# Optimization experiments

Measured on AMD Instinct MI355X. Metric: run time of the kernel, lower is better.

The kernel has to match this reference:

```python
import jax, jax.numpy as jnp
import numpy as np

N = 131072
K = 1024
D = 64

def setup_inputs() -> dict:
    key = jax.random.key(0)
    k1, k2 = jax.random.split(key)
    x = jax.random.normal(k1, (N, D), dtype=jnp.float32)
    emb_weight = jax.random.normal(k2, (K, D), dtype=jnp.float32)
    return {"x": x, "emb_weight": emb_weight}

def reference(x, emb_weight):
    distances = (
        jnp.sum(x * x, axis=1, keepdims=True)
        + jnp.sum(emb_weight * emb_weight, axis=1)
        - 2.0 * jnp.matmul(x, emb_weight.T)
    )
    codebook_indices = jnp.argmin(distances, axis=1)  # [N]
    probs = jax.nn.one_hot(codebook_indices, K, dtype=x.dtype)  # [N, K]
    z_q = emb_weight[codebook_indices]  # [N, D]
    return (z_q, probs)
```

## Files before the change

kernel.cpp:

```cpp
#include <hip/hip_runtime.h>
#include <math.h>

#define N_TOK 131072
#define K_CB  1024
#define D_DIM 64
#define MARGIN 0.0625f

#define WS_EN     0
#define WS_ES     4096
#define WS_CNT    266240
#define WS_LIST   266248

typedef short bf16x8 __attribute__((ext_vector_type(8)));
typedef float f32x4  __attribute__((ext_vector_type(4)));

__device__ __forceinline__ ushort f2bf(float f) {
    uint u = __float_as_uint(f);
    u += 0x7FFFu + ((u >> 16) & 1u);
    return (ushort)(u >> 16);
}
__device__ __forceinline__ float bf2f(ushort h) {
    return __uint_as_float(((uint)h) << 16);
}

__global__ __launch_bounds__(256) void prep_kernel(
    const float* __restrict__ emb, float* __restrict__ en,
    ushort* __restrict__ es, uint* __restrict__ fixcnt)
{
    const int tid = threadIdx.x;
    const int pb  = blockIdx.x;
    const int c6  = tid & 63;
    const int q   = tid >> 6;
    const int code = pb * 64 + c6;
    if (pb == 0 && tid == 0) *fixcnt = 0;

    const int cb = code >> 4, jj = code & 15;
    const float* er = emb + (size_t)code * D_DIM;
    #pragma unroll
    for (int j = 0; j < 16; ++j) {
        int d = q * 16 + j;
        float f = er[d];
        ushort h = f2bf(f);
        ushort l = f2bf(f - bf2f(h));
        int ks = d >> 5, quad = (d >> 3) & 3, e = d & 7;
        es[(size_t)(((cb * 4 + ks)     * 4 + quad) * 16 + jj) * 8 + e] = h;
        es[(size_t)(((cb * 4 + ks + 2) * 4 + quad) * 16 + jj) * 8 + e] = l;
    }
    if (q == 0) {
        float s = 0.f;
        #pragma unroll
        for (int d = 0; d < D_DIM; ++d) s = fmaf(er[d], er[d], s);
        en[code] = s;
    }
}

__global__ __launch_bounds__(256) void vq_onehot(
    const float* __restrict__ x, const float* __restrict__ emb,
    const float* __restrict__ en, const ushort* __restrict__ es,
    float* __restrict__ zq, float* __restrict__ probs,
    uint* __restrict__ fixcnt, uint* __restrict__ fixlist, uint fixcap)
{
    const int tid  = threadIdx.x;
    const int wave = tid >> 6, lane = tid & 63;
    const int quad = lane >> 4, l15 = lane & 15;
    const int waveRow = blockIdx.x * 128 + wave * 32;

    __shared__ int lds_bk[128];

    bf16x8 af[2][4];
    #pragma unroll
    for (int g = 0; g < 2; ++g) {
        const float* xr = x + (size_t)(waveRow + g * 16 + l15) * D_DIM + quad * 8;
        f32x4 p0 = *(const f32x4*)(xr);
        f32x4 p1 = *(const f32x4*)(xr + 4);
        f32x4 p2 = *(const f32x4*)(xr + 32);
        f32x4 p3 = *(const f32x4*)(xr + 36);
        float v0[8], v1[8];
        #pragma unroll
        for (int j = 0; j < 4; ++j) { v0[j] = p0[j]; v0[4 + j] = p1[j]; v1[j] = p2[j]; v1[4 + j] = p3[j]; }
        #pragma unroll
        for (int j = 0; j < 8; ++j) {
            ushort h0 = f2bf(v0[j]);
            af[g][0][j] = (short)h0;
            af[g][2][j] = (short)f2bf(v0[j] - bf2f(h0));
            ushort h1 = f2bf(v1[j]);
            af[g][1][j] = (short)h1;
            af[g][3][j] = (short)f2bf(v1[j] - bf2f(h1));
        }
    }

    float b1[8], b2[8]; int k1[8];
    #pragma unroll
    for (int s = 0; s < 8; ++s) { b1[s] = INFINITY; b2[s] = INFINITY; k1[s] = 0; }

    const bf16x8* __restrict__ esv = (const bf16x8*)es;
    const int fidx = quad * 16 + l15;

    bf16x8 bc[4]; float enc;
    #pragma unroll
    for (int ks = 0; ks < 4; ++ks) bc[ks] = esv[ks * 64 + fidx];
    enc = en[l15];

    #pragma unroll 2
    for (int cb = 0; cb < 64; ++cb) {
        const int nb = (cb + 1) & 63;
        bf16x8 bn[4]; float enn;
        #pragma unroll
        for (int ks = 0; ks < 4; ++ks) bn[ks] = esv[(size_t)nb * 256 + ks * 64 + fidx];
        enn = en[nb * 16 + l15];

        f32x4 acc0 = {0.f, 0.f, 0.f, 0.f};
        f32x4 acc1 = {0.f, 0.f, 0.f, 0.f};
        acc0 = __builtin_amdgcn_mfma_f32_16x16x32_bf16(af[0][0], bc[0], acc0, 0, 0, 0);
        acc0 = __builtin_amdgcn_mfma_f32_16x16x32_bf16(af[0][1], bc[1], acc0, 0, 0, 0);
        acc0 = __builtin_amdgcn_mfma_f32_16x16x32_bf16(af[0][0], bc[2], acc0, 0, 0, 0);
        acc0 = __builtin_amdgcn_mfma_f32_16x16x32_bf16(af[0][1], bc[3], acc0, 0, 0, 0);
        acc0 = __builtin_amdgcn_mfma_f32_16x16x32_bf16(af[0][2], bc[0], acc0, 0, 0, 0);
        acc0 = __builtin_amdgcn_mfma_f32_16x16x32_bf16(af[0][3], bc[1], acc0, 0, 0, 0);
        acc1 = __builtin_amdgcn_mfma_f32_16x16x32_bf16(af[1][0], bc[0], acc1, 0, 0, 0);
        acc1 = __builtin_amdgcn_mfma_f32_16x16x32_bf16(af[1][1], bc[1], acc1, 0, 0, 0);
        acc1 = __builtin_amdgcn_mfma_f32_16x16x32_bf16(af[1][0], bc[2], acc1, 0, 0, 0);
        acc1 = __builtin_amdgcn_mfma_f32_16x16x32_bf16(af[1][1], bc[3], acc1, 0, 0, 0);
        acc1 = __builtin_amdgcn_mfma_f32_16x16x32_bf16(af[1][2], bc[0], acc1, 0, 0, 0);
        acc1 = __builtin_amdgcn_mfma_f32_16x16x32_bf16(af[1][3], bc[1], acc1, 0, 0, 0);

        const int code = cb * 16 + l15;
        #pragma unroll
        for (int r = 0; r < 4; ++r) {
            {
                float d = fmaf(-2.f, acc0[r], enc);
                bool lt = d < b1[r];
                b2[r] = lt ? b1[r] : fminf(b2[r], d);
                k1[r] = lt ? code : k1[r];
                b1[r] = lt ? d : b1[r];
            }
            {
                int s = 4 + r;
                float d = fmaf(-2.f, acc1[r], enc);
                bool lt = d < b1[s];
                b2[s] = lt ? b1[s] : fminf(b2[s], d);
                k1[s] = lt ? code : k1[s];
                b1[s] = lt ? d : b1[s];
            }
        }

        #pragma unroll
        for (int ks = 0; ks < 4; ++ks) bc[ks] = bn[ks];
        enc = enn;
    }

    #pragma unroll
    for (int s = 0; s < 8; ++s) {
        #pragma unroll
        for (int off = 1; off < 16; off <<= 1) {
            float ob1 = __shfl_xor(b1[s], off);
            int   ok1 = __shfl_xor(k1[s], off);
            float ob2 = __shfl_xor(b2[s], off);
            bool better = (ob1 < b1[s]) || (ob1 == b1[s] && ok1 < k1[s]);
            float loser = better ? b1[s] : ob1;
            b1[s] = better ? ob1 : b1[s];
            k1[s] = better ? ok1 : k1[s];
            b2[s] = fminf(fminf(b2[s], ob2), loser);
        }
    }

    if (l15 == 0) {
        #pragma unroll
        for (int s = 0; s < 8; ++s) {
            int lrow = wave * 32 + (s >> 2) * 16 + quad * 4 + (s & 3);
            lds_bk[lrow] = k1[s];
            if (b2[s] - b1[s] <= MARGIN) {
                uint idx = atomicAdd(fixcnt, 1u);
                if (idx < fixcap)
                    fixlist[idx] = (uint)(blockIdx.x * 128 + lrow) | ((uint)k1[s] << 17);
            }
        }
    }

    #pragma unroll
    for (int mb = 0; mb < 8; ++mb) {
        int bk = lds_bk[wave * 32 + mb * 4 + quad];
        f32x4 v = ((const f32x4*)(emb + (size_t)bk * D_DIM))[l15];
        ((f32x4*)(zq + (size_t)(waveRow + mb * 4 + quad) * D_DIM))[l15] = v;
    }

    for (int m = 0; m < 32; ++m) {
        int bk = lds_bk[wave * 32 + m];
        float* prow = probs + (size_t)(waveRow + m) * K_CB;
        #pragma unroll
        for (int s = 0; s < 4; ++s) {
            int c = s * 256 + lane * 4;
            f32x4 v;
            v[0] = (c     == bk) ? 1.f : 0.f;
            v[1] = (c + 1 == bk) ? 1.f : 0.f;
            v[2] = (c + 2 == bk) ? 1.f : 0.f;
            v[3] = (c + 3 == bk) ? 1.f : 0.f;
            __builtin_nontemporal_store(v, (f32x4*)(prow + c));
        }
    }
}

__global__ __launch_bounds__(256) void vq_fixup(
    const float* __restrict__ x, const float* __restrict__ emb,
    const float* __restrict__ en,
    float* __restrict__ zq, float* __restrict__ probs,
    const uint* __restrict__ fixcnt, const uint* __restrict__ fixlist, uint fixcap)
{
    const int lane = threadIdx.x & 63;
    const uint gwave = (uint)((blockIdx.x * 256 + threadIdx.x) >> 6);
    uint cnt = *fixcnt;
    if (cnt > fixcap) cnt = fixcap;

    for (uint e = gwave; e < cnt; e += 1024u) {
        uint w = fixlist[e];
        int row = (int)(w & 0x1FFFFu);
        int kg  = (int)(w >> 17);
        const float* xr = x + (size_t)row * D_DIM;
        float xn = 0.f;
        #pragma unroll
        for (int d = 0; d < D_DIM; ++d) xn = fmaf(xr[d], xr[d], xn);

        float bd = INFINITY; int bk = 0;
        for (int t = 0; t < 16; ++t) {
            int code = t * 64 + lane;
            const float* er = emb + (size_t)code * D_DIM;
            float a0 = 0.f, a1 = 0.f, a2 = 0.f, a3 = 0.f;
            #pragma unroll
            for (int d = 0; d < D_DIM; d += 4) {
                a0 = fmaf(xr[d + 0], er[d + 0], a0);
                a1 = fmaf(xr[d + 1], er[d + 1], a1);
                a2 = fmaf(xr[d + 2], er[d + 2], a2);
                a3 = fmaf(xr[d + 3], er[d + 3], a3);
            }
            float acc = (a0 + a1) + (a2 + a3);
            float dist = fmaf(-2.f, acc, xn + en[code]);
            if (dist < bd) { bd = dist; bk = code; }
        }
        #pragma unroll
        for (int off = 1; off < 64; off <<= 1) {
            float od = __shfl_xor(bd, off);
            int   ok = __shfl_xor(bk, off);
            if (od < bd || (od == bd && ok < bk)) { bd = od; bk = ok; }
        }
        if (bk != kg) {
            if (lane == 0) {
                probs[(size_t)row * K_CB + kg] = 0.f;
                probs[(size_t)row * K_CB + bk] = 1.f;
            }
            if (lane < 16)
                ((f32x4*)(zq + (size_t)row * D_DIM))[lane] =
                    ((const f32x4*)(emb + (size_t)bk * D_DIM))[lane];
        }
    }
}

extern "C" void kernel_launch(void* const* d_in, const int* in_sizes, int n_in,
                              void* d_out, int out_size, void* d_ws, size_t ws_size,
                              hipStream_t stream) {
    const float* x   = (const float*)d_in[0];
    const float* emb = (const float*)d_in[1];
    float* zq    = (float*)d_out;
    float* probs = (float*)d_out + (size_t)N_TOK * D_DIM;

    char* ws = (char*)d_ws;
    float*  en      = (float*)(ws + WS_EN);
    ushort* es      = (ushort*)(ws + WS_ES);
    uint*   fixcnt  = (uint*)(ws + WS_CNT);
    uint*   fixlist = (uint*)(ws + WS_LIST);
    uint fixcap = (ws_size > WS_LIST + 4) ? (uint)((ws_size - WS_LIST) / 4) : 0u;

    prep_kernel<<<16, 256, 0, stream>>>(emb, en, es, fixcnt);
    vq_onehot<<<N_TOK / 128, 256, 0, stream>>>(x, emb, en, es, zq, probs, fixcnt, fixlist, fixcap);
    vq_fixup<<<256, 256, 0, stream>>>(x, emb, en, zq, probs, fixcnt, fixlist, fixcap);
}
```

Measured before the change: 661.2 us.

## Split one-hot probs writing into a separate streaming kernel

```diff
diff --git a/kernel.cpp b/kernel.cpp
--- a/kernel.cpp
+++ b/kernel.cpp
@@ -9,7 +9,8 @@
 #define WS_EN     0
 #define WS_ES     4096
 #define WS_CNT    266240
-#define WS_LIST   266248
+#define WS_BK     266256
+#define WS_LIST   790544
 
 typedef short bf16x8 __attribute__((ext_vector_type(8)));
 typedef float f32x4  __attribute__((ext_vector_type(4)));
@@ -54,16 +55,17 @@
     }
 }
 
-__global__ __launch_bounds__(256) void vq_onehot(
+__global__ __launch_bounds__(256) void vq_compute(
     const float* __restrict__ x, const float* __restrict__ emb,
     const float* __restrict__ en, const ushort* __restrict__ es,
-    float* __restrict__ zq, float* __restrict__ probs,
+    float* __restrict__ zq, int* __restrict__ bklist,
     uint* __restrict__ fixcnt, uint* __restrict__ fixlist, uint fixcap)
 {
     const int tid  = threadIdx.x;
     const int wave = tid >> 6, lane = tid & 63;
     const int quad = lane >> 4, l15 = lane & 15;
-    const int waveRow = blockIdx.x * 128 + wave * 32;
+    const int blockRow = blockIdx.x * 128;
+    const int waveRow  = blockRow + wave * 32;
 
     __shared__ int lds_bk[128];
 
@@ -169,10 +171,11 @@
         for (int s = 0; s < 8; ++s) {
             int lrow = wave * 32 + (s >> 2) * 16 + quad * 4 + (s & 3);
             lds_bk[lrow] = k1[s];
+            bklist[blockRow + lrow] = k1[s];
             if (b2[s] - b1[s] <= MARGIN) {
                 uint idx = atomicAdd(fixcnt, 1u);
                 if (idx < fixcap)
-                    fixlist[idx] = (uint)(blockIdx.x * 128 + lrow) | ((uint)k1[s] << 17);
+                    fixlist[idx] = (uint)(blockRow + lrow) | ((uint)k1[s] << 17);
             }
         }
     }
@@ -183,20 +186,25 @@
         f32x4 v = ((const f32x4*)(emb + (size_t)bk * D_DIM))[l15];
         ((f32x4*)(zq + (size_t)(waveRow + mb * 4 + quad) * D_DIM))[l15] = v;
     }
-
-    for (int m = 0; m < 32; ++m) {
-        int bk = lds_bk[wave * 32 + m];
-        float* prow = probs + (size_t)(waveRow + m) * K_CB;
-        #pragma unroll
-        for (int s = 0; s < 4; ++s) {
-            int c = s * 256 + lane * 4;
-            f32x4 v;
-            v[0] = (c     == bk) ? 1.f : 0.f;
-            v[1] = (c + 1 == bk) ? 1.f : 0.f;
-            v[2] = (c + 2 == bk) ? 1.f : 0.f;
-            v[3] = (c + 3 == bk) ? 1.f : 0.f;
-            __builtin_nontemporal_store(v, (f32x4*)(prow + c));
-        }
+}
+
+__global__ __launch_bounds__(256) void onehot_writer(
+    const int* __restrict__ bklist, float* __restrict__ probs)
+{
+    const int tid = threadIdx.x;
+    const int blk = blockIdx.x;
+    const int c   = tid * 4;
+    f32x4* p = (f32x4*)probs + (size_t)blk * 16384 + tid;
+    const int* bkp = bklist + blk * 64;
+    #pragma unroll
+    for (int i = 0; i < 64; ++i) {
+        const int bk = bkp[i];
+        f32x4 v;
+        v[0] = (c     == bk) ? 1.f : 0.f;
+        v[1] = (c + 1 == bk) ? 1.f : 0.f;
+        v[2] = (c + 2 == bk) ? 1.f : 0.f;
+        v[3] = (c + 3 == bk) ? 1.f : 0.f;
+        p[(size_t)i * 256] = v;
     }
 }
 
@@ -266,10 +274,12 @@
     float*  en      = (float*)(ws + WS_EN);
     ushort* es      = (ushort*)(ws + WS_ES);
     uint*   fixcnt  = (uint*)(ws + WS_CNT);
+    int*    bklist  = (int*)(ws + WS_BK);
     uint*   fixlist = (uint*)(ws + WS_LIST);
     uint fixcap = (ws_size > WS_LIST + 4) ? (uint)((ws_size - WS_LIST) / 4) : 0u;
 
     prep_kernel<<<16, 256, 0, stream>>>(emb, en, es, fixcnt);
-    vq_onehot<<<N_TOK / 128, 256, 0, stream>>>(x, emb, en, es, zq, probs, fixcnt, fixlist, fixcap);
+    vq_compute<<<N_TOK / 128, 256, 0, stream>>>(x, emb, en, es, zq, bklist, fixcnt, fixlist, fixcap);
+    onehot_writer<<<N_TOK / 64, 256, 0, stream>>>(bklist, probs);
     vq_fixup<<<256, 256, 0, stream>>>(x, emb, en, zq, probs, fixcnt, fixlist, fixcap);
 }
```

New measurement: 699.3 us. 1.06x slower.

## Split codebook across wave pairs and vectorize fixup distance search

Applied to the files above, without the earlier changes.

```diff
diff --git a/kernel.cpp b/kernel.cpp
--- a/kernel.cpp
+++ b/kernel.cpp
@@ -4,12 +4,12 @@
 #define N_TOK 131072
 #define K_CB  1024
 #define D_DIM 64
-#define MARGIN 0.0625f
+#define MARGIN 0.03f
 
 #define WS_EN     0
 #define WS_ES     4096
 #define WS_CNT    266240
-#define WS_LIST   266248
+#define WS_LIST   266256
 
 typedef short bf16x8 __attribute__((ext_vector_type(8)));
 typedef float f32x4  __attribute__((ext_vector_type(4)));
@@ -63,14 +63,20 @@
     const int tid  = threadIdx.x;
     const int wave = tid >> 6, lane = tid & 63;
     const int quad = lane >> 4, l15 = lane & 15;
-    const int waveRow = blockIdx.x * 128 + wave * 32;
-
-    __shared__ int lds_bk[128];
+    const int rg = wave >> 1;
+    const int h  = wave & 1;
+    const int blockRow = blockIdx.x * 64;
+    const int waveRowBase = blockRow + rg * 32;
+
+    __shared__ float lds_b1[2][64];
+    __shared__ float lds_b2[2][64];
+    __shared__ int   lds_k1[2][64];
+    __shared__ int   lds_bk[64];
 
     bf16x8 af[2][4];
     #pragma unroll
     for (int g = 0; g < 2; ++g) {
-        const float* xr = x + (size_t)(waveRow + g * 16 + l15) * D_DIM + quad * 8;
+        const float* xr = x + (size_t)(waveRowBase + g * 16 + l15) * D_DIM + quad * 8;
         f32x4 p0 = *(const f32x4*)(xr);
         f32x4 p1 = *(const f32x4*)(xr + 4);
         f32x4 p2 = *(const f32x4*)(xr + 32);
@@ -95,19 +101,21 @@
 
     const bf16x8* __restrict__ esv = (const bf16x8*)es;
     const int fidx = quad * 16 + l15;
+    const int cb0  = h * 32;
 
     bf16x8 bc[4]; float enc;
     #pragma unroll
-    for (int ks = 0; ks < 4; ++ks) bc[ks] = esv[ks * 64 + fidx];
-    enc = en[l15];
+    for (int ks = 0; ks < 4; ++ks) bc[ks] = esv[(size_t)cb0 * 256 + ks * 64 + fidx];
+    enc = en[cb0 * 16 + l15];
 
     #pragma unroll 2
-    for (int cb = 0; cb < 64; ++cb) {
-        const int nb = (cb + 1) & 63;
+    for (int i = 0; i < 32; ++i) {
+        const int cb  = cb0 + i;
+        const int nbi = cb0 + ((i + 1) & 31);
         bf16x8 bn[4]; float enn;
         #pragma unroll
-        for (int ks = 0; ks < 4; ++ks) bn[ks] = esv[(size_t)nb * 256 + ks * 64 + fidx];
-        enn = en[nb * 16 + l15];
+        for (int ks = 0; ks < 4; ++ks) bn[ks] = esv[(size_t)nbi * 256 + ks * 64 + fidx];
+        enn = en[nbi * 16 + l15];
 
         f32x4 acc0 = {0.f, 0.f, 0.f, 0.f};
         f32x4 acc1 = {0.f, 0.f, 0.f, 0.f};
@@ -167,26 +175,42 @@
     if (l15 == 0) {
         #pragma unroll
         for (int s = 0; s < 8; ++s) {
-            int lrow = wave * 32 + (s >> 2) * 16 + quad * 4 + (s & 3);
-            lds_bk[lrow] = k1[s];
-            if (b2[s] - b1[s] <= MARGIN) {
-                uint idx = atomicAdd(fixcnt, 1u);
-                if (idx < fixcap)
-                    fixlist[idx] = (uint)(blockIdx.x * 128 + lrow) | ((uint)k1[s] << 17);
-            }
-        }
-    }
-
-    #pragma unroll
-    for (int mb = 0; mb < 8; ++mb) {
-        int bk = lds_bk[wave * 32 + mb * 4 + quad];
+            int idx = rg * 32 + (s >> 2) * 16 + quad * 4 + (s & 3);
+            lds_b1[h][idx] = b1[s];
+            lds_b2[h][idx] = b2[s];
+            lds_k1[h][idx] = k1[s];
+        }
+    }
+    __syncthreads();
+
+    if (tid < 64) {
+        float a1 = lds_b1[0][tid], a2 = lds_b2[0][tid]; int ak = lds_k1[0][tid];
+        float c1 = lds_b1[1][tid], c2 = lds_b2[1][tid]; int ck = lds_k1[1][tid];
+        bool bwin = c1 < a1;
+        float m1 = bwin ? c1 : a1;
+        int   mk = bwin ? ck : ak;
+        float loser = bwin ? a1 : c1;
+        float m2 = fminf(fminf(a2, c2), loser);
+        lds_bk[tid] = mk;
+        if (m2 - m1 <= MARGIN) {
+            uint idx = atomicAdd(fixcnt, 1u);
+            if (idx < fixcap) fixlist[idx] = (uint)(blockRow + tid) | ((uint)mk << 17);
+        }
+    }
+    __syncthreads();
+
+    #pragma unroll
+    for (int mb = 0; mb < 4; ++mb) {
+        int rl = wave * 16 + mb * 4 + quad;
+        int bk = lds_bk[rl];
         f32x4 v = ((const f32x4*)(emb + (size_t)bk * D_DIM))[l15];
-        ((f32x4*)(zq + (size_t)(waveRow + mb * 4 + quad) * D_DIM))[l15] = v;
-    }
-
-    for (int m = 0; m < 32; ++m) {
-        int bk = lds_bk[wave * 32 + m];
-        float* prow = probs + (size_t)(waveRow + m) * K_CB;
+        ((f32x4*)(zq + (size_t)(blockRow + rl) * D_DIM))[l15] = v;
+    }
+
+    for (int m = 0; m < 16; ++m) {
+        int rl = wave * 16 + m;
+        int bk = lds_bk[rl];
+        float* prow = probs + (size_t)(blockRow + rl) * K_CB;
         #pragma unroll
         for (int s = 0; s < 4; ++s) {
             int c = s * 256 + lane * 4;
@@ -195,7 +219,7 @@
             v[1] = (c + 1 == bk) ? 1.f : 0.f;
             v[2] = (c + 2 == bk) ? 1.f : 0.f;
             v[3] = (c + 3 == bk) ? 1.f : 0.f;
-            __builtin_nontemporal_store(v, (f32x4*)(prow + c));
+            *(f32x4*)(prow + c) = v;
         }
     }
 }
@@ -207,6 +231,7 @@
     const uint* __restrict__ fixcnt, const uint* __restrict__ fixlist, uint fixcap)
 {
     const int lane = threadIdx.x & 63;
+    const int quad = lane >> 4, l15 = lane & 15;
     const uint gwave = (uint)((blockIdx.x * 256 + threadIdx.x) >> 6);
     uint cnt = *fixcnt;
     if (cnt > fixcap) cnt = fixcap;
@@ -215,29 +240,37 @@
         uint w = fixlist[e];
         int row = (int)(w & 0x1FFFFu);
         int kg  = (int)(w >> 17);
-        const float* xr = x + (size_t)row * D_DIM;
+
+        const f32x4* xr4 = (const f32x4*)(x + (size_t)row * D_DIM) + quad * 4;
+        f32x4 xv[4];
+        #pragma unroll
+        for (int c = 0; c < 4; ++c) xv[c] = xr4[c];
         float xn = 0.f;
         #pragma unroll
-        for (int d = 0; d < D_DIM; ++d) xn = fmaf(xr[d], xr[d], xn);
+        for (int c = 0; c < 4; ++c)
+            #pragma unroll
+            for (int j = 0; j < 4; ++j) xn = fmaf(xv[c][j], xv[c][j], xn);
+        xn += __shfl_xor(xn, 16);
+        xn += __shfl_xor(xn, 32);
 
         float bd = INFINITY; int bk = 0;
-        for (int t = 0; t < 16; ++t) {
-            int code = t * 64 + lane;
-            const float* er = emb + (size_t)code * D_DIM;
-            float a0 = 0.f, a1 = 0.f, a2 = 0.f, a3 = 0.f;
+        for (int t = 0; t < 64; ++t) {
+            int code = t * 16 + l15;
+            const f32x4* er4 = (const f32x4*)(emb + (size_t)code * D_DIM) + quad * 4;
+            float dot = 0.f;
             #pragma unroll
-            for (int d = 0; d < D_DIM; d += 4) {
-                a0 = fmaf(xr[d + 0], er[d + 0], a0);
-                a1 = fmaf(xr[d + 1], er[d + 1], a1);
-                a2 = fmaf(xr[d + 2], er[d + 2], a2);
-                a3 = fmaf(xr[d + 3], er[d + 3], a3);
+            for (int c = 0; c < 4; ++c) {
+                f32x4 ev = er4[c];
+                #pragma unroll
+                for (int j = 0; j < 4; ++j) dot = fmaf(xv[c][j], ev[j], dot);
             }
-            float acc = (a0 + a1) + (a2 + a3);
-            float dist = fmaf(-2.f, acc, xn + en[code]);
+            dot += __shfl_xor(dot, 16);
+            dot += __shfl_xor(dot, 32);
+            float dist = fmaf(-2.f, dot, xn + en[code]);
             if (dist < bd) { bd = dist; bk = code; }
         }
         #pragma unroll
-        for (int off = 1; off < 64; off <<= 1) {
+        for (int off = 1; off < 16; off <<= 1) {
             float od = __shfl_xor(bd, off);
             int   ok = __shfl_xor(bk, off);
             if (od < bd || (od == bd && ok < bk)) { bd = od; bk = ok; }
@@ -270,6 +303,6 @@
     uint fixcap = (ws_size > WS_LIST + 4) ? (uint)((ws_size - WS_LIST) / 4) : 0u;
 
     prep_kernel<<<16, 256, 0, stream>>>(emb, en, es, fixcnt);
-    vq_onehot<<<N_TOK / 128, 256, 0, stream>>>(x, emb, en, es, zq, probs, fixcnt, fixlist, fixcap);
+    vq_onehot<<<N_TOK / 64, 256, 0, stream>>>(x, emb, en, es, zq, probs, fixcnt, fixlist, fixcap);
     vq_fixup<<<256, 256, 0, stream>>>(x, emb, en, zq, probs, fixcnt, fixlist, fixcap);
 }
```

Measured after the change: 623.4 us. 1.06x faster.
